# Kernel tuning notes

Measured on AMD Instinct MI355X. Metric: run time of the kernel, lower is better.

The kernel has to match this reference:

```python
import jax, jax.numpy as jnp
import numpy as np

B, N, F, H, C, HID = 2, 2048, 64, 4, 32, 128
HIN = H * C  # 128, GAT output width (concat heads)


def setup_inputs() -> dict:
    key = jax.random.key(0)
    ks = jax.random.split(key, 16)
    glorot = jax.nn.initializers.glorot_normal()
    x = jax.random.normal(ks[0], (B, N, F), jnp.float32)
    a = (jax.random.uniform(ks[1], (B, N, N)) < 0.01).astype(jnp.float32)
    a = jnp.maximum(a, jnp.eye(N, dtype=jnp.float32)[None])
    h = jax.random.normal(ks[2], (B, N, HID), jnp.float32)
    # GATConv params (spektral batch mode, concat_heads=True)
    kernel = glorot(ks[3], (F, H, C), jnp.float32)
    attn_self = glorot(ks[4], (H, C), jnp.float32)
    attn_nei = glorot(ks[5], (H, C), jnp.float32)
    bias_gat = jnp.zeros((HIN,), jnp.float32)
    # GRU-style gate params
    b_u = glorot(ks[6], (N, 1), jnp.float32)
    b_r = glorot(ks[7], (N, 1), jnp.float32)
    b_c = glorot(ks[8], (N, 1), jnp.float32)
    W_u = glorot(ks[9], (HID + HIN, HID), jnp.float32)
    W_r = glorot(ks[10], (HID + HIN, HID), jnp.float32)
    W_c = glorot(ks[11], (HID + HIN, HID), jnp.float32)
    # bilinear decoder (p) weight
    R_p = glorot(ks[12], (HID, HID), jnp.float32)
    return {"x": x, "a": a, "h": h, "kernel": kernel, "attn_self": attn_self,
            "attn_nei": attn_nei, "bias_gat": bias_gat, "b_u": b_u, "b_r": b_r,
            "b_c": b_c, "W_u": W_u, "W_r": W_r, "W_c": W_c, "R_p": R_p}


def _gat(x, a, kernel, attn_self, attn_nei, bias_gat):
    # x: [B,N,F] -> per-head features xp: [B,N,H,C]
    xp = jnp.einsum('bnf,fhc->bnhc', x, kernel)
    es = jnp.einsum('bnhc,hc->bnh', xp, attn_self)   # target score
    en = jnp.einsum('bnhc,hc->bnh', xp, attn_nei)    # source score
    # e[b,i,j,h] = leakyrelu(es_i + en_j), masked by adjacency
    e = jax.nn.leaky_relu(es[:, :, None, :] + en[:, None, :, :], 0.2)
    e = e + (-1e9) * (1.0 - a)[..., None]
    alpha = jax.nn.softmax(e, axis=2)                # softmax over sources j
    out = jnp.einsum('bijh,bjhc->bihc', alpha, xp)   # aggregate
    return out.reshape(out.shape[0], out.shape[1], -1) + bias_gat  # [B,N,H*C]


def reference(x, a, h, kernel, attn_self, attn_nei, bias_gat,
              b_u, b_r, b_c, W_u, W_r, W_c, R_p):
    conv_u = _gat(x, a, kernel, attn_self, attn_nei, bias_gat)  # [B,N,HIN]
    z = jnp.concatenate([conv_u, h], axis=-1)                    # [B,N,HIN+HID]
    u = jax.nn.sigmoid(b_u + z @ W_u)                            # b_u [N,1] broadcasts
    r = jax.nn.sigmoid(b_r + z @ W_r)
    zc = jnp.concatenate([conv_u, r * h], axis=-1)
    c = jnp.tanh(b_c + zc @ W_c)
    h_prime = u * h + (1.0 - u) * c                              # [B,N,HID]
    A = jnp.einsum('bnh,hk,bmk->bnm', h_prime, R_p, h_prime)     # bilinear decode [B,N,N]
    return A, h_prime
```

## Files before the change

### kernel.cpp

```cpp
#include <hip/hip_runtime.h>
#include <hip/hip_bf16.h>
#include <math.h>

#define NB 2
#define NN 2048
#define FD 64
#define NH 4
#define HIDD 128
#define ROWS_TOT (NB*NN)

#define XP_OFF   0
#define ES_OFF   524288
#define EN_OFF   540672
#define CU_OFF   557056
#define TBF_OFF  1081344
#define HPBF_OFF 1343488

#define A_ELEMS (NB*NN*NN)

typedef __attribute__((ext_vector_type(8))) short bf16x8;
typedef __attribute__((ext_vector_type(8))) unsigned short ushort8;
typedef __attribute__((ext_vector_type(4))) float f32x4;

__global__ __launch_bounds__(256) void k1_xp(
    const float* __restrict__ x, const float* __restrict__ kern,
    const float* __restrict__ as_, const float* __restrict__ an_,
    float* __restrict__ xp, float* __restrict__ es, float* __restrict__ en)
{
  __shared__ float xr[8][FD];
  const int t = threadIdx.x;
  const int col = t & 127, rg = t >> 7;
  const int row0 = blockIdx.x * 8;
  for (int idx = t; idx < 8*FD; idx += 256)
    xr[idx >> 6][idx & 63] = x[(size_t)row0*FD + idx];
  __syncthreads();
  const float asv = as_[col], anv = an_[col];
  float acc[4] = {0.f, 0.f, 0.f, 0.f};
  for (int f = 0; f < FD; ++f) {
    const float kv = kern[f*128 + col];
#pragma unroll
    for (int rr = 0; rr < 4; ++rr)
      acc[rr] = fmaf(xr[rg*4 + rr][f], kv, acc[rr]);
  }
  const int h = col >> 5;
  const int c = col & 31;
#pragma unroll
  for (int rr = 0; rr < 4; ++rr) {
    const int grow = row0 + rg*4 + rr;
    xp[(size_t)grow*128 + col] = acc[rr];
    float s = acc[rr]*asv, n_ = acc[rr]*anv;
#pragma unroll
    for (int mk = 16; mk >= 1; mk >>= 1) {
      s  += __shfl_xor(s,  mk, 32);
      n_ += __shfl_xor(n_, mk, 32);
    }
    if (c == 0) { es[grow*NH + h] = s; en[grow*NH + h] = n_; }
  }
}

__global__ __launch_bounds__(256) void k2_attn(
    const float* __restrict__ a, const float* __restrict__ xp,
    const float* __restrict__ es, const float* __restrict__ en,
    const float* __restrict__ bias, float* __restrict__ cu)
{
  __shared__ unsigned short sidx[4][NN];
  __shared__ float swl[4][64][NH];
  const int t = threadIdx.x;
  const int ln = t & 63, wv = t >> 6;
  const int row = blockIdx.x * 4 + wv;
  const int b = row >> 11;
  const float4 esi = *(const float4*)(es + (size_t)row*NH);

  int deg = 0;
  const float4* arow4 = (const float4*)(a + (size_t)row*NN);
#pragma unroll
  for (int cch = 0; cch < 8; ++cch) {
    const float4 v = arow4[cch*64 + ln];
    const int j0 = cch*256 + ln*4;
    const float vv[4] = {v.x, v.y, v.z, v.w};
#pragma unroll
    for (int q = 0; q < 4; ++q) {
      const unsigned long long m = __ballot(vv[q] > 0.5f);
      if (vv[q] > 0.5f) {
        const int pos = deg + (int)__popcll(m & ((1ull << ln) - 1ull));
        sidx[wv][pos] = (unsigned short)(j0 + q);
      }
      deg += (int)__popcll(m);
    }
  }

  const int col0 = ln, col1 = ln + 64;
  const int h0 = ln >> 5;
  float m0=-1e30f, m1=-1e30f, m2=-1e30f, m3=-1e30f;
  float s0=0.f, s1=0.f, s2=0.f, s3=0.f;
  float acc0=0.f, acc1=0.f;
  for (int base = 0; base < deg; base += 64) {
    const int rem = min(64, deg - base);
    float t0=-1e30f, t1=-1e30f, t2=-1e30f, t3=-1e30f;
    if (ln < rem) {
      const int j = sidx[wv][base + ln];
      const float4 e4 = *(const float4*)(en + (size_t)(b*NN + j)*NH);
      t0 = esi.x + e4.x; t0 = t0 > 0.f ? t0 : 0.2f*t0;
      t1 = esi.y + e4.y; t1 = t1 > 0.f ? t1 : 0.2f*t1;
      t2 = esi.z + e4.z; t2 = t2 > 0.f ? t2 : 0.2f*t2;
      t3 = esi.w + e4.w; t3 = t3 > 0.f ? t3 : 0.2f*t3;
    }
    float c0=t0, c1=t1, c2=t2, c3=t3;
#pragma unroll
    for (int mk = 32; mk >= 1; mk >>= 1) {
      c0 = fmaxf(c0, __shfl_xor(c0, mk));
      c1 = fmaxf(c1, __shfl_xor(c1, mk));
      c2 = fmaxf(c2, __shfl_xor(c2, mk));
      c3 = fmaxf(c3, __shfl_xor(c3, mk));
    }
    const float nm0 = fmaxf(m0,c0), nm1 = fmaxf(m1,c1);
    const float nm2 = fmaxf(m2,c2), nm3 = fmaxf(m3,c3);
    const float r0 = expf(m0-nm0), r1 = expf(m1-nm1);
    const float r2 = expf(m2-nm2), r3 = expf(m3-nm3);
    s0 *= r0; s1 *= r1; s2 *= r2; s3 *= r3;
    float w0=0.f, w1=0.f, w2=0.f, w3=0.f;
    if (ln < rem) {
      w0 = expf(t0-nm0); w1 = expf(t1-nm1);
      w2 = expf(t2-nm2); w3 = expf(t3-nm3);
    }
    float u0=w0, u1=w1, u2=w2, u3=w3;
#pragma unroll
    for (int mk = 32; mk >= 1; mk >>= 1) {
      u0 += __shfl_xor(u0, mk);
      u1 += __shfl_xor(u1, mk);
      u2 += __shfl_xor(u2, mk);
      u3 += __shfl_xor(u3, mk);
    }
    s0 += u0; s1 += u1; s2 += u2; s3 += u3;
    acc0 *= (h0 ? r1 : r0);
    acc1 *= (h0 ? r3 : r2);
    swl[wv][ln][0] = w0; swl[wv][ln][1] = w1;
    swl[wv][ln][2] = w2; swl[wv][ln][3] = w3;
#pragma unroll 4
    for (int k = 0; k < rem; ++k) {
      const int j = sidx[wv][base + k];
      const float* xr = xp + (size_t)(b*NN + j)*128;
      acc0 = fmaf(swl[wv][k][h0],     xr[col0], acc0);
      acc1 = fmaf(swl[wv][k][2 + h0], xr[col1], acc1);
    }
    m0=nm0; m1=nm1; m2=nm2; m3=nm3;
  }
  const float den0 = h0 ? s1 : s0;
  const float den1 = h0 ? s3 : s2;
  cu[(size_t)row*128 + col0] = acc0/den0 + bias[col0];
  cu[(size_t)row*128 + col1] = acc1/den1 + bias[col1];
}

__global__ __launch_bounds__(512) void k3_gate(
    const float* __restrict__ cu_, const float* __restrict__ hin,
    const float* __restrict__ bu, const float* __restrict__ br,
    const float* __restrict__ bc, const float* __restrict__ Wu,
    const float* __restrict__ Wr, const float* __restrict__ Wc,
    const float* __restrict__ Rp, float* __restrict__ hp_out,
    __hip_bfloat16* __restrict__ hp_bf, __hip_bfloat16* __restrict__ t_bf)
{
  __shared__ float zT[256][17];
  __shared__ float rhT[128][17];
  __shared__ float hpL[16][128];
  const int t = threadIdx.x;
  const int col = t & 127, rg = t >> 7;
  const int row0 = blockIdx.x * 16;
  for (int idx = t; idx < 16*256; idx += 512) {
    const int r = idx >> 8, d = idx & 255;
    zT[d][r] = (d < 128) ? cu_[(size_t)(row0+r)*128 + d]
                         : hin[(size_t)(row0+r)*128 + (d-128)];
  }
  __syncthreads();
  float au[4] = {0.f,0.f,0.f,0.f}, ar[4] = {0.f,0.f,0.f,0.f};
  for (int d = 0; d < 256; ++d) {
    const float wu = Wu[d*128 + col];
    const float wr = Wr[d*128 + col];
#pragma unroll
    for (int rr = 0; rr < 4; ++rr) {
      const float z = zT[d][rg*4 + rr];
      au[rr] = fmaf(z, wu, au[rr]);
      ar[rr] = fmaf(z, wr, ar[rr]);
    }
  }
  float uu[4], hv[4];
#pragma unroll
  for (int rr = 0; rr < 4; ++rr) {
    const int r = rg*4 + rr;
    const int n = (row0 + r) & (NN-1);
    hv[rr] = zT[128 + col][r];
    uu[rr] = 1.f/(1.f + expf(-(bu[n] + au[rr])));
    const float rv = 1.f/(1.f + expf(-(br[n] + ar[rr])));
    rhT[col][r] = rv * hv[rr];
  }
  __syncthreads();
  float ac[4] = {0.f,0.f,0.f,0.f};
  for (int d = 0; d < 128; ++d) {
    const float wc1 = Wc[d*128 + col];
    const float wc2 = Wc[(128 + d)*128 + col];
#pragma unroll
    for (int rr = 0; rr < 4; ++rr) {
      ac[rr] = fmaf(zT[d][rg*4+rr],  wc1, ac[rr]);
      ac[rr] = fmaf(rhT[d][rg*4+rr], wc2, ac[rr]);
    }
  }
#pragma unroll
  for (int rr = 0; rr < 4; ++rr) {
    const int r = rg*4 + rr;
    const int grow = row0 + r;
    const int n = grow & (NN-1);
    const float cc = tanhf(bc[n] + ac[rr]);
    const float hpv = uu[rr]*hv[rr] + (1.f - uu[rr])*cc;
    hp_out[(size_t)grow*128 + col] = hpv;
    hp_bf[(size_t)grow*128 + col] = __float2bfloat16(hpv);
    hpL[r][col] = hpv;
  }
  __syncthreads();
  float tacc[4] = {0.f,0.f,0.f,0.f};
  for (int d = 0; d < 128; ++d) {
    const float rv = Rp[d*128 + col];
#pragma unroll
    for (int rr = 0; rr < 4; ++rr)
      tacc[rr] = fmaf(hpL[rg*4+rr][d], rv, tacc[rr]);
  }
#pragma unroll
  for (int rr = 0; rr < 4; ++rr)
    t_bf[(size_t)(row0 + rg*4 + rr)*128 + col] = __float2bfloat16(tacc[rr]);
}

__global__ __launch_bounds__(256) void k4b_dec(
    const __hip_bfloat16* __restrict__ t_bf,
    const __hip_bfloat16* __restrict__ hp_bf,
    float* __restrict__ A)
{
  __shared__ __align__(16) char Alds[128*256];
  __shared__ __align__(16) char Blds[128*256];
  const int t = threadIdx.x;
  const int ln = t & 63, wv = t >> 6;
  const int b = blockIdx.z;
  const int i0 = blockIdx.y * 128, j0 = blockIdx.x * 128;

  {
    const int sub = ln >> 4;
    const int cb  = (ln & 15) * 16;
#pragma unroll
    for (int q = 0; q < 8; ++q) {
      const int chunk = wv*8 + q;
      const int row = chunk*4 + sub;
      const int scb = cb ^ ((row & 7) << 4);
      const ushort8 va = *(const ushort8*)
          ((const char*)(t_bf + ((size_t)(b*NN) + i0 + row)*128) + cb);
      *(ushort8*)(Alds + row*256 + scb) = va;
      const ushort8 vb = *(const ushort8*)
          ((const char*)(hp_bf + ((size_t)(b*NN) + j0 + row)*128) + cb);
      *(ushort8*)(Blds + row*256 + scb) = vb;
    }
  }
  __syncthreads();

  const int wr = wv >> 1, wc = wv & 1;
  const int lrow = ln & 15;
  const int kid  = ln >> 4;
  f32x4 acc[4][4];
  const f32x4 zero = {0.f, 0.f, 0.f, 0.f};
#pragma unroll
  for (int m = 0; m < 4; ++m)
#pragma unroll
    for (int n = 0; n < 4; ++n) acc[m][n] = zero;

#pragma unroll
  for (int ks = 0; ks < 4; ++ks) {
    const int kb = ks*64 + kid*16;
    bf16x8 af[4], bfr[4];
#pragma unroll
    for (int m = 0; m < 4; ++m) {
      const int arow = wr*64 + m*16 + lrow;
      af[m] = *(const bf16x8*)(Alds + arow*256 + (kb ^ ((arow & 7) << 4)));
      const int brow = wc*64 + m*16 + lrow;
      bfr[m] = *(const bf16x8*)(Blds + brow*256 + (kb ^ ((brow & 7) << 4)));
    }
#pragma unroll
    for (int m = 0; m < 4; ++m)
#pragma unroll
      for (int n = 0; n < 4; ++n)
        acc[m][n] = __builtin_amdgcn_mfma_f32_16x16x32_bf16(
            af[m], bfr[n], acc[m][n], 0, 0, 0);
  }

#pragma unroll
  for (int m = 0; m < 4; ++m) {
    const int grow = i0 + wr*64 + m*16 + (ln >> 4)*4;
#pragma unroll
    for (int n = 0; n < 4; ++n) {
      const int gcol = j0 + wc*64 + n*16 + (ln & 15);
      float* Ap = A + ((size_t)b*NN + grow)*NN + gcol;
#pragma unroll
      for (int r = 0; r < 4; ++r)
        Ap[(size_t)r*NN] = acc[m][n][r];
    }
  }
}

extern "C" void kernel_launch(void* const* d_in, const int* in_sizes, int n_in,
                              void* d_out, int out_size, void* d_ws, size_t ws_size,
                              hipStream_t stream)
{
  const float* x    = (const float*)d_in[0];
  const float* a    = (const float*)d_in[1];
  const float* h    = (const float*)d_in[2];
  const float* kern = (const float*)d_in[3];
  const float* as_  = (const float*)d_in[4];
  const float* an_  = (const float*)d_in[5];
  const float* bias = (const float*)d_in[6];
  const float* bu   = (const float*)d_in[7];
  const float* br   = (const float*)d_in[8];
  const float* bc   = (const float*)d_in[9];
  const float* Wu   = (const float*)d_in[10];
  const float* Wr   = (const float*)d_in[11];
  const float* Wc   = (const float*)d_in[12];
  const float* Rp   = (const float*)d_in[13];
  (void)in_sizes; (void)n_in; (void)out_size; (void)ws_size;

  float* ws = (float*)d_ws;
  float* xp = ws + XP_OFF;
  float* es = ws + ES_OFF;
  float* en = ws + EN_OFF;
  float* cu = ws + CU_OFF;
  __hip_bfloat16* t_bf  = (__hip_bfloat16*)(ws + TBF_OFF);
  __hip_bfloat16* hp_bf = (__hip_bfloat16*)(ws + HPBF_OFF);

  float* A  = (float*)d_out;
  float* hp = (float*)d_out + A_ELEMS;

  hipLaunchKernelGGL(k1_xp,   dim3(ROWS_TOT/8), dim3(256), 0, stream,
                     x, kern, as_, an_, xp, es, en);
  hipLaunchKernelGGL(k2_attn, dim3(ROWS_TOT/4), dim3(256), 0, stream,
                     a, xp, es, en, bias, cu);
  hipLaunchKernelGGL(k3_gate, dim3(ROWS_TOT/16), dim3(512), 0, stream,
                     cu, h, bu, br, bc, Wu, Wr, Wc, Rp, hp, hp_bf, t_bf);
  hipLaunchKernelGGL(k4b_dec, dim3(NN/128, NN/128, NB), dim3(256), 0, stream,
                     t_bf, hp_bf, A);
}
```

Before: 162.8 us.

## Move GRU gate and decoder projection GEMMs to split-bf16 MFMA

Replaces the scalar FP32 gate kernel with an MFMA version. Activations and weights are split into bf16 hi/lo pairs and combined with three MFMAs per tile to keep near-FP32 accuracy. A new prep kernel converts and transposes the weights on every call. It also vectorises the xp projection kernel to use float4 columns per thread, which shortens the shuffle reduction. In exchange it adds an extra launch and triples the MFMA work to compensate for precision.

New measurement: 153.3 us. 5.8% less time.

```diff
diff --git a/kernel.cpp b/kernel.cpp
--- a/kernel.cpp
+++ b/kernel.cpp
@@ -15,12 +15,61 @@
 #define CU_OFF   557056
 #define TBF_OFF  1081344
 #define HPBF_OFF 1343488
+#define WUH_OFF  1605632
+#define WUL_OFF  1622016
+#define WRH_OFF  1638400
+#define WRL_OFF  1654784
+#define WCH_OFF  1671168
+#define WCL_OFF  1687552
+#define RPH_OFF  1703936
+#define RPL_OFF  1712128
 
 #define A_ELEMS (NB*NN*NN)
 
 typedef __attribute__((ext_vector_type(8))) short bf16x8;
 typedef __attribute__((ext_vector_type(8))) unsigned short ushort8;
+typedef __attribute__((ext_vector_type(4))) unsigned short ushort4v;
 typedef __attribute__((ext_vector_type(4))) float f32x4;
+
+#define MFMA_BF16(a,b,c) __builtin_amdgcn_mfma_f32_16x16x32_bf16((a),(b),(c),0,0,0)
+
+static __device__ inline unsigned short f2bf(float x) {
+  __hip_bfloat16 b = __float2bfloat16(x);
+  unsigned short u; __builtin_memcpy(&u, &b, 2); return u;
+}
+static __device__ inline float bf2f(unsigned short u) {
+  __hip_bfloat16 b; __builtin_memcpy(&b, &u, 2); return __bfloat162float(b);
+}
+static __device__ inline void split2(float x, unsigned short& hi, unsigned short& lo) {
+  hi = f2bf(x);
+  lo = f2bf(x - bf2f(hi));
+}
+
+__global__ __launch_bounds__(256) void k0_prep(
+    const float* __restrict__ Wu, const float* __restrict__ Wr,
+    const float* __restrict__ Wc, const float* __restrict__ Rp,
+    unsigned short* __restrict__ wuh, unsigned short* __restrict__ wul,
+    unsigned short* __restrict__ wrh, unsigned short* __restrict__ wrl,
+    unsigned short* __restrict__ wch, unsigned short* __restrict__ wcl,
+    unsigned short* __restrict__ rph, unsigned short* __restrict__ rpl)
+{
+  const int gid = blockIdx.x*256 + threadIdx.x;
+  if (gid < 98304) {
+    const int which = gid >> 15;
+    const int loc = gid & 32767;
+    const int j = loc >> 8, k = loc & 255;
+    const float* W = which == 0 ? Wu : (which == 1 ? Wr : Wc);
+    unsigned short* oh = which == 0 ? wuh : (which == 1 ? wrh : wch);
+    unsigned short* ol = which == 0 ? wul : (which == 1 ? wrl : wcl);
+    unsigned short h, l; split2(W[k*128 + j], h, l);
+    oh[loc] = h; ol[loc] = l;
+  } else if (gid < 114688) {
+    const int loc = gid - 98304;
+    const int j = loc >> 7, k = loc & 127;
+    unsigned short h, l; split2(Rp[k*128 + j], h, l);
+    rph[loc] = h; rpl[loc] = l;
+  }
+}
 
 __global__ __launch_bounds__(256) void k1_xp(
     const float* __restrict__ x, const float* __restrict__ kern,
@@ -29,32 +78,35 @@
 {
   __shared__ float xr[8][FD];
   const int t = threadIdx.x;
-  const int col = t & 127, rg = t >> 7;
   const int row0 = blockIdx.x * 8;
   for (int idx = t; idx < 8*FD; idx += 256)
     xr[idx >> 6][idx & 63] = x[(size_t)row0*FD + idx];
   __syncthreads();
-  const float asv = as_[col], anv = an_[col];
-  float acc[4] = {0.f, 0.f, 0.f, 0.f};
+  const int c4 = (t & 31) * 4;
+  const int rq = t >> 5;
+  const float4 asv = *(const float4*)(as_ + c4);
+  const float4 anv = *(const float4*)(an_ + c4);
+  float4 acc = make_float4(0.f, 0.f, 0.f, 0.f);
   for (int f = 0; f < FD; ++f) {
-    const float kv = kern[f*128 + col];
-#pragma unroll
-    for (int rr = 0; rr < 4; ++rr)
-      acc[rr] = fmaf(xr[rg*4 + rr][f], kv, acc[rr]);
-  }
-  const int h = col >> 5;
-  const int c = col & 31;
-#pragma unroll
-  for (int rr = 0; rr < 4; ++rr) {
-    const int grow = row0 + rg*4 + rr;
-    xp[(size_t)grow*128 + col] = acc[rr];
-    float s = acc[rr]*asv, n_ = acc[rr]*anv;
-#pragma unroll
-    for (int mk = 16; mk >= 1; mk >>= 1) {
-      s  += __shfl_xor(s,  mk, 32);
-      n_ += __shfl_xor(n_, mk, 32);
-    }
-    if (c == 0) { es[grow*NH + h] = s; en[grow*NH + h] = n_; }
+    const float4 kv = *(const float4*)(kern + f*128 + c4);
+    const float xv = xr[rq][f];
+    acc.x = fmaf(xv, kv.x, acc.x);
+    acc.y = fmaf(xv, kv.y, acc.y);
+    acc.z = fmaf(xv, kv.z, acc.z);
+    acc.w = fmaf(xv, kv.w, acc.w);
+  }
+  const int grow = row0 + rq;
+  *(float4*)(xp + (size_t)grow*128 + c4) = acc;
+  float s  = acc.x*asv.x + acc.y*asv.y + acc.z*asv.z + acc.w*asv.w;
+  float n_ = acc.x*anv.x + acc.y*anv.y + acc.z*anv.z + acc.w*anv.w;
+#pragma unroll
+  for (int mk = 4; mk >= 1; mk >>= 1) {
+    s  += __shfl_xor(s,  mk, 64);
+    n_ += __shfl_xor(n_, mk, 64);
+  }
+  if ((t & 7) == 0) {
+    const int h = (t & 31) >> 3;
+    es[grow*NH + h] = s; en[grow*NH + h] = n_;
   }
 }
 
@@ -151,80 +203,164 @@
   cu[(size_t)row*128 + col1] = acc1/den1 + bias[col1];
 }
 
-__global__ __launch_bounds__(512) void k3_gate(
+__global__ __launch_bounds__(256) void k3_mfma(
     const float* __restrict__ cu_, const float* __restrict__ hin,
     const float* __restrict__ bu, const float* __restrict__ br,
-    const float* __restrict__ bc, const float* __restrict__ Wu,
-    const float* __restrict__ Wr, const float* __restrict__ Wc,
-    const float* __restrict__ Rp, float* __restrict__ hp_out,
+    const float* __restrict__ bc,
+    const unsigned short* __restrict__ wuh, const unsigned short* __restrict__ wul,
+    const unsigned short* __restrict__ wrh, const unsigned short* __restrict__ wrl,
+    const unsigned short* __restrict__ wch, const unsigned short* __restrict__ wcl,
+    const unsigned short* __restrict__ rph, const unsigned short* __restrict__ rpl,
+    float* __restrict__ hp_out,
     __hip_bfloat16* __restrict__ hp_bf, __hip_bfloat16* __restrict__ t_bf)
 {
-  __shared__ float zT[256][17];
-  __shared__ float rhT[128][17];
-  __shared__ float hpL[16][128];
+  __shared__ __align__(16) char zH[16*512];
+  __shared__ __align__(16) char zL[16*512];
+  __shared__ __align__(16) char rhH[16*256];
+  __shared__ __align__(16) char rhL[16*256];
+  __shared__ __align__(16) char hpH[16*256];
+  __shared__ __align__(16) char hpLo[16*256];
   const int t = threadIdx.x;
-  const int col = t & 127, rg = t >> 7;
   const int row0 = blockIdx.x * 16;
-  for (int idx = t; idx < 16*256; idx += 512) {
-    const int r = idx >> 8, d = idx & 255;
-    zT[d][r] = (d < 128) ? cu_[(size_t)(row0+r)*128 + d]
-                         : hin[(size_t)(row0+r)*128 + (d-128)];
+
+#pragma unroll
+  for (int i = 0; i < 4; ++i) {
+    const int q = t + 256*i;
+    const int r = q >> 6;
+    const int c = (q & 63) * 4;
+    float4 v;
+    if (c < 128) v = *(const float4*)(cu_ + (size_t)(row0+r)*128 + c);
+    else         v = *(const float4*)(hin + (size_t)(row0+r)*128 + (c-128));
+    unsigned short hx, lx, hy, ly, hz, lz, hw, lw;
+    split2(v.x, hx, lx); split2(v.y, hy, ly);
+    split2(v.z, hz, lz); split2(v.w, hw, lw);
+    ushort4v h4; h4[0]=hx; h4[1]=hy; h4[2]=hz; h4[3]=hw;
+    ushort4v l4; l4[0]=lx; l4[1]=ly; l4[2]=lz; l4[3]=lw;
+    const int byte = (c*2) ^ ((r & 7) << 4);
+    *(ushort4v*)(zH + r*512 + byte) = h4;
+    *(ushort4v*)(zL + r*512 + byte) = l4;
   }
   __syncthreads();
-  float au[4] = {0.f,0.f,0.f,0.f}, ar[4] = {0.f,0.f,0.f,0.f};
-  for (int d = 0; d < 256; ++d) {
-    const float wu = Wu[d*128 + col];
-    const float wr = Wr[d*128 + col];
-#pragma unroll
-    for (int rr = 0; rr < 4; ++rr) {
-      const float z = zT[d][rg*4 + rr];
-      au[rr] = fmaf(z, wu, au[rr]);
-      ar[rr] = fmaf(z, wr, ar[rr]);
-    }
-  }
-  float uu[4], hv[4];
-#pragma unroll
-  for (int rr = 0; rr < 4; ++rr) {
-    const int r = rg*4 + rr;
-    const int n = (row0 + r) & (NN-1);
-    hv[rr] = zT[128 + col][r];
-    uu[rr] = 1.f/(1.f + expf(-(bu[n] + au[rr])));
-    const float rv = 1.f/(1.f + expf(-(br[n] + ar[rr])));
-    rhT[col][r] = rv * hv[rr];
+
+  const int ln = t & 63, wv = t >> 6;
+  const int n0 = wv * 32;
+  const int lr = ln & 15, kid = ln >> 4;
+  const int sw = (lr & 7) << 4;
+  const f32x4 zero = {0.f, 0.f, 0.f, 0.f};
+
+  f32x4 accU[2] = {zero, zero}, accR[2] = {zero, zero};
+#pragma unroll
+  for (int ks = 0; ks < 8; ++ks) {
+    const int kb = ks*64 + kid*16;
+    const bf16x8 ah = *(const bf16x8*)(zH + lr*512 + (kb ^ sw));
+    const bf16x8 al = *(const bf16x8*)(zL + lr*512 + (kb ^ sw));
+#pragma unroll
+    for (int nt = 0; nt < 2; ++nt) {
+      const int j = n0 + nt*16 + lr;
+      const bf16x8 buH = *(const bf16x8*)((const char*)wuh + j*512 + kb);
+      const bf16x8 buL = *(const bf16x8*)((const char*)wul + j*512 + kb);
+      const bf16x8 brH = *(const bf16x8*)((const char*)wrh + j*512 + kb);
+      const bf16x8 brL = *(const bf16x8*)((const char*)wrl + j*512 + kb);
+      accU[nt] = MFMA_BF16(ah, buH, accU[nt]);
+      accU[nt] = MFMA_BF16(ah, buL, accU[nt]);
+      accU[nt] = MFMA_BF16(al, buH, accU[nt]);
+      accR[nt] = MFMA_BF16(ah, brH, accR[nt]);
+      accR[nt] = MFMA_BF16(ah, brL, accR[nt]);
+      accR[nt] = MFMA_BF16(al, brH, accR[nt]);
+    }
+  }
+
+  float hval[2][4], uval[2][4];
+#pragma unroll
+  for (int nt = 0; nt < 2; ++nt) {
+    const int colg = n0 + nt*16 + lr;
+#pragma unroll
+    for (int reg = 0; reg < 4; ++reg) {
+      const int row16 = kid*4 + reg;
+      const int grow = row0 + row16;
+      const int nrow = grow & (NN-1);
+      const float h_ = hin[(size_t)grow*128 + colg];
+      const float uv = 1.f/(1.f + expf(-(bu[nrow] + accU[nt][reg])));
+      const float rv = 1.f/(1.f + expf(-(br[nrow] + accR[nt][reg])));
+      hval[nt][reg] = h_; uval[nt][reg] = uv;
+      unsigned short hs, ls; split2(rv * h_, hs, ls);
+      const int byte = (colg*2) ^ ((row16 & 7) << 4);
+      *(unsigned short*)(rhH + row16*256 + byte) = hs;
+      *(unsigned short*)(rhL + row16*256 + byte) = ls;
+    }
   }
   __syncthreads();
-  float ac[4] = {0.f,0.f,0.f,0.f};
-  for (int d = 0; d < 128; ++d) {
-    const float wc1 = Wc[d*128 + col];
-    const float wc2 = Wc[(128 + d)*128 + col];
-#pragma unroll
-    for (int rr = 0; rr < 4; ++rr) {
-      ac[rr] = fmaf(zT[d][rg*4+rr],  wc1, ac[rr]);
-      ac[rr] = fmaf(rhT[d][rg*4+rr], wc2, ac[rr]);
-    }
-  }
-#pragma unroll
-  for (int rr = 0; rr < 4; ++rr) {
-    const int r = rg*4 + rr;
-    const int grow = row0 + r;
-    const int n = grow & (NN-1);
-    const float cc = tanhf(bc[n] + ac[rr]);
-    const float hpv = uu[rr]*hv[rr] + (1.f - uu[rr])*cc;
-    hp_out[(size_t)grow*128 + col] = hpv;
-    hp_bf[(size_t)grow*128 + col] = __float2bfloat16(hpv);
-    hpL[r][col] = hpv;
+
+  f32x4 accC[2] = {zero, zero};
+#pragma unroll
+  for (int ks = 0; ks < 8; ++ks) {
+    const int kb = ks*64 + kid*16;
+    bf16x8 ah, al;
+    if (ks < 4) {
+      ah = *(const bf16x8*)(zH + lr*512 + (kb ^ sw));
+      al = *(const bf16x8*)(zL + lr*512 + (kb ^ sw));
+    } else {
+      const int kb2 = (ks-4)*64 + kid*16;
+      ah = *(const bf16x8*)(rhH + lr*256 + (kb2 ^ sw));
+      al = *(const bf16x8*)(rhL + lr*256 + (kb2 ^ sw));
+    }
+#pragma unroll
+    for (int nt = 0; nt < 2; ++nt) {
+      const int j = n0 + nt*16 + lr;
+      const bf16x8 bH = *(const bf16x8*)((const char*)wch + j*512 + kb);
+      const bf16x8 bL = *(const bf16x8*)((const char*)wcl + j*512 + kb);
+      accC[nt] = MFMA_BF16(ah, bH, accC[nt]);
+      accC[nt] = MFMA_BF16(ah, bL, accC[nt]);
+      accC[nt] = MFMA_BF16(al, bH, accC[nt]);
+    }
+  }
+
+#pragma unroll
+  for (int nt = 0; nt < 2; ++nt) {
+    const int colg = n0 + nt*16 + lr;
+#pragma unroll
+    for (int reg = 0; reg < 4; ++reg) {
+      const int row16 = kid*4 + reg;
+      const int grow = row0 + row16;
+      const int nrow = grow & (NN-1);
+      const float cc = tanhf(bc[nrow] + accC[nt][reg]);
+      const float uv = uval[nt][reg];
+      const float hpv = uv*hval[nt][reg] + (1.f - uv)*cc;
+      hp_out[(size_t)grow*128 + colg] = hpv;
+      hp_bf[(size_t)grow*128 + colg] = __float2bfloat16(hpv);
+      unsigned short hs, ls; split2(hpv, hs, ls);
+      const int byte = (colg*2) ^ ((row16 & 7) << 4);
+      *(unsigned short*)(hpH  + row16*256 + byte) = hs;
+      *(unsigned short*)(hpLo + row16*256 + byte) = ls;
+    }
   }
   __syncthreads();
-  float tacc[4] = {0.f,0.f,0.f,0.f};
-  for (int d = 0; d < 128; ++d) {
-    const float rv = Rp[d*128 + col];
-#pragma unroll
-    for (int rr = 0; rr < 4; ++rr)
-      tacc[rr] = fmaf(hpL[rg*4+rr][d], rv, tacc[rr]);
-  }
-#pragma unroll
-  for (int rr = 0; rr < 4; ++rr)
-    t_bf[(size_t)(row0 + rg*4 + rr)*128 + col] = __float2bfloat16(tacc[rr]);
+
+  f32x4 accT[2] = {zero, zero};
+#pragma unroll
+  for (int ks = 0; ks < 4; ++ks) {
+    const int kb = ks*64 + kid*16;
+    const bf16x8 ah = *(const bf16x8*)(hpH  + lr*256 + (kb ^ sw));
+    const bf16x8 al = *(const bf16x8*)(hpLo + lr*256 + (kb ^ sw));
+#pragma unroll
+    for (int nt = 0; nt < 2; ++nt) {
+      const int j = n0 + nt*16 + lr;
+      const bf16x8 bH = *(const bf16x8*)((const char*)rph + j*256 + kb);
+      const bf16x8 bL = *(const bf16x8*)((const char*)rpl + j*256 + kb);
+      accT[nt] = MFMA_BF16(ah, bH, accT[nt]);
+      accT[nt] = MFMA_BF16(ah, bL, accT[nt]);
+      accT[nt] = MFMA_BF16(al, bH, accT[nt]);
+    }
+  }
+#pragma unroll
+  for (int nt = 0; nt < 2; ++nt) {
+    const int colg = n0 + nt*16 + lr;
+#pragma unroll
+    for (int reg = 0; reg < 4; ++reg) {
+      const int grow = row0 + kid*4 + reg;
+      t_bf[(size_t)grow*128 + colg] = __float2bfloat16(accT[nt][reg]);
+    }
+  }
 }
 
 __global__ __launch_bounds__(256) void k4b_dec(
@@ -282,8 +418,7 @@
     for (int m = 0; m < 4; ++m)
 #pragma unroll
       for (int n = 0; n < 4; ++n)
-        acc[m][n] = __builtin_amdgcn_mfma_f32_16x16x32_bf16(
-            af[m], bfr[n], acc[m][n], 0, 0, 0);
+        acc[m][n] = MFMA_BF16(af[m], bfr[n], acc[m][n]);
   }
 
 #pragma unroll
@@ -327,16 +462,27 @@
   float* cu = ws + CU_OFF;
   __hip_bfloat16* t_bf  = (__hip_bfloat16*)(ws + TBF_OFF);
   __hip_bfloat16* hp_bf = (__hip_bfloat16*)(ws + HPBF_OFF);
+  unsigned short* wuh = (unsigned short*)(ws + WUH_OFF);
+  unsigned short* wul = (unsigned short*)(ws + WUL_OFF);
+  unsigned short* wrh = (unsigned short*)(ws + WRH_OFF);
+  unsigned short* wrl = (unsigned short*)(ws + WRL_OFF);
+  unsigned short* wch = (unsigned short*)(ws + WCH_OFF);
+  unsigned short* wcl = (unsigned short*)(ws + WCL_OFF);
+  unsigned short* rph = (unsigned short*)(ws + RPH_OFF);
+  unsigned short* rpl = (unsigned short*)(ws + RPL_OFF);
 
   float* A  = (float*)d_out;
   float* hp = (float*)d_out + A_ELEMS;
 
+  hipLaunchKernelGGL(k0_prep, dim3(448), dim3(256), 0, stream,
+                     Wu, Wr, Wc, Rp, wuh, wul, wrh, wrl, wch, wcl, rph, rpl);
   hipLaunchKernelGGL(k1_xp,   dim3(ROWS_TOT/8), dim3(256), 0, stream,
                      x, kern, as_, an_, xp, es, en);
   hipLaunchKernelGGL(k2_attn, dim3(ROWS_TOT/4), dim3(256), 0, stream,
                      a, xp, es, en, bias, cu);
-  hipLaunchKernelGGL(k3_gate, dim3(ROWS_TOT/16), dim3(512), 0, stream,
-                     cu, h, bu, br, bc, Wu, Wr, Wc, Rp, hp, hp_bf, t_bf);
+  hipLaunchKernelGGL(k3_mfma, dim3(ROWS_TOT/16), dim3(256), 0, stream,
+                     cu, h, bu, br, bc, wuh, wul, wrh, wrl, wch, wcl, rph, rpl,
+                     hp, hp_bf, t_bf);
   hipLaunchKernelGGL(k4b_dec, dim3(NN/128, NN/128, NB), dim3(256), 0, stream,
                      t_bf, hp_bf, A);
 }
```
